# Performance work log

Measured on AMD Instinct MI355X. Metric: run time of the kernel, lower is better.

Reference implementation:

```python
import jax, jax.numpy as jnp
import numpy as np

MID = 16
HEADS = 8
HEAD_DIM = MID // HEADS  # 2
EPS = 1e-5


def posembed(length, dim):
    # get_posembed_linear: sin-cos 1D positional embedding
    pos = jnp.arange(length, dtype=jnp.float32)
    omega = jnp.arange(dim // 2, dtype=jnp.float32) / (dim / 2.0)
    omega = 1.0 / (10000.0 ** omega)
    out = pos[:, None] * omega[None, :]  # [L, dim//2]
    return jnp.concatenate([jnp.sin(out), jnp.cos(out)], axis=1)  # [L, dim]


def layernorm(x, g, b):
    m = x.mean(-1, keepdims=True)
    v = ((x - m) ** 2).mean(-1, keepdims=True)
    return (x - m) * jax.lax.rsqrt(v + EPS) * g + b


def conv2d(x, w, b):
    # NCHW 3x3 SAME conv
    y = jax.lax.conv_general_dilated(x, w, (1, 1), 'SAME',
                                     dimension_numbers=('NCHW', 'OIHW', 'NCHW'))
    return y + b[None, :, None, None]


def attention(x, wq, wk, wv, wo, bo):
    # diffusers Attention: self-attn, no qkv bias, out bias
    B, S, C = x.shape
    q = (x @ wq.T).reshape(B, S, HEADS, HEAD_DIM)
    k = (x @ wk.T).reshape(B, S, HEADS, HEAD_DIM)
    v = (x @ wv.T).reshape(B, S, HEADS, HEAD_DIM)
    scale = 1.0 / np.sqrt(HEAD_DIM).astype(np.float32)
    scores = jnp.einsum('bshd,bthd->bhst', q, k) * scale
    p = jax.nn.softmax(scores, axis=-1)
    o = jnp.einsum('bhst,bthd->bshd', p, v).reshape(B, S, C)
    return o @ wo.T + bo


def setup_inputs() -> dict:
    key = jax.random.key(0)
    ks = jax.random.split(key, 24)

    def n(k, shape, s=0.05):
        return jax.random.normal(k, shape, dtype=jnp.float32) * s

    b, f, h, w, c = 2, 16, 64, 64, 16
    inp = {
        'hidden_states': n(ks[0], (b, f, h, w, c), 1.0),
        'ref_stats': n(ks[1], (b, f, h, w, c), 1.0),
        'emb': n(ks[2], (b, 512), 1.0),
        'conv_in_w': n(ks[3], (MID, c, 3, 3)),
        'conv_in_b': jnp.zeros((MID,), jnp.float32),
        'emb1_w': n(ks[4], (MID, 512)),
        'emb1_b': jnp.zeros((MID,), jnp.float32),
        'emb2_w': n(ks[5], (MID, MID)),
        'emb2_b': jnp.zeros((MID,), jnp.float32),
        'wqx': n(ks[6], (MID, MID)), 'wkx': n(ks[7], (MID, MID)),
        'wvx': n(ks[8], (MID, MID)), 'wox': n(ks[9], (MID, MID)),
        'box': jnp.zeros((MID,), jnp.float32),
        'wqy': n(ks[10], (MID, MID)), 'wky': n(ks[11], (MID, MID)),
        'wvy': n(ks[12], (MID, MID)), 'woy': n(ks[13], (MID, MID)),
        'boy': jnp.zeros((MID,), jnp.float32),
        'wqt': n(ks[14], (MID, MID)), 'wkt': n(ks[15], (MID, MID)),
        'wvt': n(ks[16], (MID, MID)), 'wot': n(ks[17], (MID, MID)),
        'bot': jnp.zeros((MID,), jnp.float32),
        'norm_g': jnp.ones((MID,), jnp.float32),
        'norm_b': jnp.zeros((MID,), jnp.float32),
        'proj_w': n(ks[18], (c, MID, 3, 3)),  # zero_module in torch; random here so grads flow
        'proj_b': jnp.zeros((c,), jnp.float32),
    }
    return inp


def reference(hidden_states, ref_stats, emb,
              conv_in_w, conv_in_b, emb1_w, emb1_b, emb2_w, emb2_b,
              wqx, wkx, wvx, wox, box,
              wqy, wky, wvy, woy, boy,
              wqt, wkt, wvt, wot, bot,
              norm_g, norm_b, proj_w, proj_b):
    b, f, h, w, c = hidden_states.shape

    # conv stem on (b f) c h w
    x = hidden_states.reshape(b * f, h, w, c).transpose(0, 3, 1, 2)
    x = conv2d(x, conv_in_w, conv_in_b)
    r = ref_stats.reshape(b * f, h, w, c).transpose(0, 3, 1, 2)
    r = conv2d(r, conv_in_w, conv_in_b)

    # TimestepEmbedding: linear -> silu -> linear, broadcast over frames/HW
    e = jax.nn.silu(emb @ emb1_w.T + emb1_b) @ emb2_w.T + emb2_b  # [b, MID]
    r = r + jnp.repeat(e, f, axis=0)[:, :, None, None]

    hs = x.reshape(b, f, MID, h, w).transpose(0, 1, 3, 4, 2)  # b f h w c
    rs = r.reshape(b, f, MID, h, w).transpose(0, 1, 3, 4, 2)

    # row (x) attention: cat along w -> (b f h) 2w c
    cat = jnp.concatenate([hs, rs], axis=3).reshape(b * f * h, 2 * w, MID)
    pe = posembed(2 * w, MID)
    resx = attention(layernorm(cat + pe[None], norm_g, norm_b), wqx, wkx, wvx, wox, box)
    resx = resx[:, :w].reshape(b, f, h, w, MID)

    # column (y) attention: cat along h -> (b f w) 2h c
    cat = jnp.concatenate([resx, rs], axis=2)            # b f 2h w c
    cat = cat.transpose(0, 1, 3, 2, 4).reshape(b * f * w, 2 * h, MID)
    pe = posembed(2 * h, MID)
    resy = attention(layernorm(cat + pe[None], norm_g, norm_b), wqy, wky, wvy, woy, boy)
    resy = resy[:, :h].reshape(b, f, w, h, MID).transpose(0, 1, 3, 2, 4)

    # temporal (t) attention: cat along f -> (b h w) 2f c
    cat = jnp.concatenate([resy, rs], axis=1)            # b 2f h w c
    cat = cat.transpose(0, 2, 3, 1, 4).reshape(b * h * w, 2 * f, MID)
    pe = posembed(2 * f, MID)
    rest = attention(layernorm(cat + pe[None], norm_g, norm_b), wqt, wkt, wvt, wot, bot)
    rest = rest[:, :f].reshape(b, h, w, f, MID).transpose(0, 3, 4, 1, 2).reshape(b * f, MID, h, w)

    out = conv2d(rest, proj_w, proj_b)  # (b f) c h w
    return hidden_states + out.reshape(b, f, c, h, w).transpose(0, 1, 3, 4, 2)
```

## Files before the change

### kernel.cpp

```cpp
#include <hip/hip_runtime.h>
#include <hip/hip_bf16.h>

typedef __hip_bfloat16 bf16;

__device__ __forceinline__ float b2f(bf16 x) { return __bfloat162float(x); }

#define BB   2
#define FF   16
#define HH   64
#define WW   64
#define CC   16
#define NIMG (BB*FF)
#define PIX  (HH*WW)
#define IMGSZ (PIX*CC)

#define QSCALE_LOG2E 1.0201394f

__device__ __forceinline__ void ld16bf(const bf16* p, float* x) {
    const uint4* p4 = reinterpret_cast<const uint4*>(p);
    uint4 u0 = p4[0], u1 = p4[1];
    unsigned uu[8] = {u0.x, u0.y, u0.z, u0.w, u1.x, u1.y, u1.z, u1.w};
    #pragma unroll
    for (int k = 0; k < 8; ++k) {
        union { unsigned u; float f; } lo, hi;
        lo.u = uu[k] << 16;
        hi.u = uu[k] & 0xffff0000u;
        x[2 * k] = lo.f;
        x[2 * k + 1] = hi.f;
    }
}
__device__ __forceinline__ void st16bf(bf16* p, const float* x) {
    union { bf16 h[16]; uint4 u[2]; } o;
    #pragma unroll
    for (int k = 0; k < 16; ++k) o.h[k] = __float2bfloat16(x[k]);
    uint4* p4 = reinterpret_cast<uint4*>(p);
    p4[0] = o.u[0];
    p4[1] = o.u[1];
}

__device__ __forceinline__ void ld16f(const float* p, float* x) {
    const float4* p4 = reinterpret_cast<const float4*>(p);
    #pragma unroll
    for (int q = 0; q < 4; ++q) {
        float4 v = p4[q];
        x[4 * q] = v.x; x[4 * q + 1] = v.y; x[4 * q + 2] = v.z; x[4 * q + 3] = v.w;
    }
}
__device__ __forceinline__ void st16f(float* p, const float* x) {
    float4* p4 = reinterpret_cast<float4*>(p);
    #pragma unroll
    for (int q = 0; q < 4; ++q)
        p4[q] = make_float4(x[4 * q], x[4 * q + 1], x[4 * q + 2], x[4 * q + 3]);
}

__device__ __forceinline__ unsigned packbf2(float a, float b) {
    union { bf16 h[2]; unsigned u; } pk;
    pk.h[0] = __float2bfloat16(a);
    pk.h[1] = __float2bfloat16(b);
    return pk.u;
}

__global__ __launch_bounds__(256) void conv_in_kernel(
    const float* __restrict__ hid, const float* __restrict__ ref,
    const float* __restrict__ cw, const float* __restrict__ cb,
    const float* __restrict__ emb,
    const float* __restrict__ e1w, const float* __restrict__ e1b,
    const float* __restrict__ e2w, const float* __restrict__ e2b,
    bf16* __restrict__ A, bf16* __restrict__ R)
{
    __shared__ float wl[9 * 256];
    __shared__ float bl[16];
    __shared__ float hl[16];
    __shared__ float el[16];
    int t = threadIdx.x;
    {
        int ic = t >> 4, oc = t & 15;
        #pragma unroll
        for (int k = 0; k < 9; ++k)
            wl[k * 256 + t] = cw[(oc * 16 + ic) * 9 + k];
    }
    if (t < 16) bl[t] = cb[t];

    int gid  = blockIdx.x * 256 + t;
    int wi   = gid & 63;
    int hi   = (gid >> 6) & 63;
    int img2 = gid >> 12;
    int isref = img2 >> 5;
    int img  = img2 & 31;
    int bi   = img >> 4;

    if (isref) {
        if (t < 16) {
            float acc = e1b[t];
            const float* er = emb + bi * 512;
            const float* wr = e1w + t * 512;
            for (int k = 0; k < 512; ++k) acc = fmaf(er[k], wr[k], acc);
            hl[t] = acc / (1.f + __expf(-acc));
        }
        __syncthreads();
        if (t < 16) {
            float acc = e2b[t];
            #pragma unroll
            for (int k = 0; k < 16; ++k) acc = fmaf(hl[k], e2w[t * 16 + k], acc);
            el[t] = acc;
        }
    }
    __syncthreads();

    const float* inp = (isref ? ref : hid) + (size_t)img * IMGSZ;
    float acc[16];
    #pragma unroll
    for (int oc = 0; oc < 16; ++oc)
        acc[oc] = bl[oc] + (isref ? el[oc] : 0.f);

    for (int ky = 0; ky < 3; ++ky) {
        int y = hi + ky - 1;
        if ((unsigned)y >= 64u) continue;
        for (int kx = 0; kx < 3; ++kx) {
            int x = wi + kx - 1;
            if ((unsigned)x >= 64u) continue;
            float xv[16];
            ld16f(inp + (((y << 6) + x) << 4), xv);
            const float* wt = &wl[(ky * 3 + kx) * 256];
            #pragma unroll
            for (int ic = 0; ic < 16; ++ic) {
                #pragma unroll
                for (int oc = 0; oc < 16; ++oc)
                    acc[oc] = fmaf(xv[ic], wt[ic * 16 + oc], acc[oc]);
            }
        }
    }
    bf16* op = (isref ? R : A) + ((size_t)(img * PIX + (hi << 6) + wi) << 4);
    st16bf(op, acc);
}

template<int S, int SEQPB>
__global__ __launch_bounds__(256, 5) void attn_kernel(
    bf16* __restrict__ A, const bf16* __restrict__ R,
    int d2, int str1, int str2, int tokStride,
    const float* __restrict__ wq, const float* __restrict__ wk,
    const float* __restrict__ wv, const float* __restrict__ wo,
    const float* __restrict__ bo, const float* __restrict__ gw,
    const float* __restrict__ bw)
{
    constexpr int HS = S / 2;
    constexpr int KQ = S / 2;
    constexpr int ITEMS = 256 / SEQPB;
    constexpr int KROW = 20;
    constexpr int QROW = 20;

    __shared__ float wql[256], wkl[256], wvl[256], wolT[256];
    __shared__ float bol[16], gl[16], blw[16];
    __shared__ __align__(16) float kL[SEQPB * S * KROW];
    __shared__ __align__(16) float vL[SEQPB * S * KROW];
    __shared__ __align__(16) float qoL[SEQPB * HS * QROW];
    __shared__ int   bases[SEQPB];

    int t = threadIdx.x;
    wql[t] = wq[t] * QSCALE_LOG2E;
    wkl[t] = wk[t];
    wvl[t] = wv[t];
    wolT[(t & 15) * 16 + (t >> 4)] = wo[t];
    if (t < 16) { bol[t] = bo[t]; gl[t] = gw[t]; blw[t] = bw[t]; }
    if (t < SEQPB) {
        int seq = blockIdx.x * SEQPB + t;
        bases[t] = (seq / d2) * str1 + (seq % d2) * str2;
    }
    __syncthreads();

    {
        int pair = t >> 1, halfT = t & 1;
        int sq = pair / S, i = pair % S;
        const bf16* src = (i < HS)
            ? (A + bases[sq] + (size_t)i * tokStride)
            : (R + bases[sq] + (size_t)(i - HS) * tokStride);
        float x[16];
        ld16bf(src, x);
        const float om[8] = {1.f, 0.31622776601683794f, 0.1f, 0.031622776601683794f,
                             0.01f, 0.0031622776601683794f, 0.001f, 0.00031622776601683794f};
        float fi = (float)i;
        #pragma unroll
        for (int k = 0; k < 8; ++k) {
            float a = fi * om[k];
            x[k]     += __sinf(a);
            x[k + 8] += __cosf(a);
        }
        float m = 0.f;
        #pragma unroll
        for (int c = 0; c < 16; ++c) m += x[c];
        m *= (1.f / 16.f);
        float var = 0.f;
        #pragma unroll
        for (int c = 0; c < 16; ++c) { float d = x[c] - m; var = fmaf(d, d, var); }
        var *= (1.f / 16.f);
        float rs = rsqrtf(var + 1e-5f);
        float xn[16];
        #pragma unroll
        for (int c = 0; c < 16; ++c) xn[c] = (x[c] - m) * rs * gl[c] + blw[c];

        int db = halfT * 8;
        float qv[8], kv[8], vv[8];
        #pragma unroll
        for (int dd = 0; dd < 8; ++dd) {
            int d = db + dd;
            float aq = 0.f, ak = 0.f, av = 0.f;
            #pragma unroll
            for (int c = 0; c < 16; ++c) {
                aq = fmaf(xn[c], wql[d * 16 + c], aq);
                ak = fmaf(xn[c], wkl[d * 16 + c], ak);
                av = fmaf(xn[c], wvl[d * 16 + c], av);
            }
            qv[dd] = aq; kv[dd] = ak; vv[dd] = av;
        }
        float* kr = &kL[(sq * S + i) * KROW + db];
        float* vr = &vL[(sq * S + i) * KROW + db];
        reinterpret_cast<float4*>(kr)[0] = make_float4(kv[0], kv[1], kv[2], kv[3]);
        reinterpret_cast<float4*>(kr)[1] = make_float4(kv[4], kv[5], kv[6], kv[7]);
        reinterpret_cast<float4*>(vr)[0] = make_float4(vv[0], vv[1], vv[2], vv[3]);
        reinterpret_cast<float4*>(vr)[1] = make_float4(vv[4], vv[5], vv[6], vv[7]);
        if (i < HS) {
            float* qrow = &qoL[(sq * HS + i) * QROW + db];
            reinterpret_cast<float4*>(qrow)[0] = make_float4(qv[0], qv[1], qv[2], qv[3]);
            reinterpret_cast<float4*>(qrow)[1] = make_float4(qv[4], qv[5], qv[6], qv[7]);
        }
    }
    __syncthreads();

    int sq2 = t / ITEMS;
    int r   = t % ITEMS;
    int qg  = r >> 4;
    int hd  = (r >> 1) & 7;
    int half = r & 1;
    {
        float q0[4], q1[4], l[4], a0[4], a1[4];
        #pragma unroll
        for (int qq = 0; qq < 4; ++qq) {
            float2 qv = *reinterpret_cast<const float2*>(
                &qoL[(sq2 * HS + qg * 4 + qq) * QROW + 2 * hd]);
            q0[qq] = qv.x;
            q1[qq] = qv.y;
            l[qq] = 0.f; a0[qq] = 0.f; a1[qq] = 0.f;
        }
        const float* kp = &kL[(sq2 * S + half) * KROW + 2 * hd];
        const float* vp = &vL[(sq2 * S + half) * KROW + 2 * hd];
        #pragma unroll
        for (int jj = 0; jj < KQ; ++jj) {
            float2 kj = *reinterpret_cast<const float2*>(kp + jj * 2 * KROW);
            float2 vj = *reinterpret_cast<const float2*>(vp + jj * 2 * KROW);
            #pragma unroll
            for (int qq = 0; qq < 4; ++qq) {
                float s = fmaf(q0[qq], kj.x, q1[qq] * kj.y);
                float p = __builtin_amdgcn_exp2f(s);
                l[qq] += p;
                a0[qq] = fmaf(p, vj.x, a0[qq]);
                a1[qq] = fmaf(p, vj.y, a1[qq]);
            }
        }
        #pragma unroll
        for (int qq = 0; qq < 4; ++qq) {
            l[qq]  += __shfl_xor(l[qq], 1);
            a0[qq] += __shfl_xor(a0[qq], 1);
            a1[qq] += __shfl_xor(a1[qq], 1);
        }
        __syncthreads();
        if (half == 0) {
            #pragma unroll
            for (int qq = 0; qq < 4; ++qq) {
                float inv = 1.f / l[qq];
                *reinterpret_cast<float2*>(
                    &qoL[(sq2 * HS + qg * 4 + qq) * QROW + 2 * hd]) =
                    make_float2(a0[qq] * inv, a1[qq] * inv);
            }
        }
    }
    __syncthreads();

    #pragma unroll
    for (int rep = 0; rep < 2; ++rep) {
        int idx = t + rep * 256;
        int sq3 = idx / (HS * 8);
        int rr  = idx % (HS * 8);
        int tok = rr >> 3;
        int cp  = rr & 7;
        const float* orow = &qoL[(sq3 * HS + tok) * QROW];
        float acc0 = bol[2 * cp], acc1 = bol[2 * cp + 1];
        #pragma unroll
        for (int d = 0; d < 16; ++d) {
            acc0 = fmaf(orow[d], wolT[d * 16 + 2 * cp], acc0);
            acc1 = fmaf(orow[d], wolT[d * 16 + 2 * cp + 1], acc1);
        }
        *reinterpret_cast<unsigned*>(
            A + bases[sq3] + (size_t)tok * tokStride + 2 * cp) =
            packbf2(acc0, acc1);
    }
}

__global__ __launch_bounds__(256) void conv_out_kernel(
    const bf16* __restrict__ A, const float* __restrict__ hid,
    const float* __restrict__ pw, const float* __restrict__ pb,
    float* __restrict__ out)
{
    __shared__ float wl[9 * 256];
    __shared__ float bl[16];
    int t = threadIdx.x;
    {
        int ic = t >> 4, oc = t & 15;
        #pragma unroll
        for (int k = 0; k < 9; ++k)
            wl[k * 256 + t] = pw[(oc * 16 + ic) * 9 + k];
    }
    if (t < 16) bl[t] = pb[t];
    __syncthreads();

    int gid = blockIdx.x * 256 + t;
    int wi = gid & 63, hi = (gid >> 6) & 63;
    int img = gid >> 12;
    const bf16* inp = A + ((size_t)img << 16);
    float acc[16];
    #pragma unroll
    for (int oc = 0; oc < 16; ++oc) acc[oc] = bl[oc];

    for (int ky = 0; ky < 3; ++ky) {
        int y = hi + ky - 1;
        if ((unsigned)y >= 64u) continue;
        for (int kx = 0; kx < 3; ++kx) {
            int x = wi + kx - 1;
            if ((unsigned)x >= 64u) continue;
            float xv[16];
            ld16bf(inp + (((y << 6) + x) << 4), xv);
            const float* wt = &wl[(ky * 3 + kx) * 256];
            #pragma unroll
            for (int ic = 0; ic < 16; ++ic) {
                #pragma unroll
                for (int oc = 0; oc < 16; ++oc)
                    acc[oc] = fmaf(xv[ic], wt[ic * 16 + oc], acc[oc]);
            }
        }
    }
    size_t off = ((size_t)gid) << 4;
    float hv[16];
    ld16f(hid + off, hv);
    float res[16];
    #pragma unroll
    for (int k = 0; k < 16; ++k) res[k] = acc[k] + hv[k];
    st16f(out + off, res);
}

extern "C" void kernel_launch(void* const* d_in, const int* in_sizes, int n_in,
                              void* d_out, int out_size, void* d_ws, size_t ws_size,
                              hipStream_t stream) {
    const float* hid  = (const float*)d_in[0];
    const float* ref  = (const float*)d_in[1];
    const float* emb  = (const float*)d_in[2];
    const float* ciw  = (const float*)d_in[3];
    const float* cib  = (const float*)d_in[4];
    const float* e1w  = (const float*)d_in[5];
    const float* e1b  = (const float*)d_in[6];
    const float* e2w  = (const float*)d_in[7];
    const float* e2b  = (const float*)d_in[8];
    const float* wqx  = (const float*)d_in[9];
    const float* wkx  = (const float*)d_in[10];
    const float* wvx  = (const float*)d_in[11];
    const float* wox  = (const float*)d_in[12];
    const float* box_ = (const float*)d_in[13];
    const float* wqy  = (const float*)d_in[14];
    const float* wky  = (const float*)d_in[15];
    const float* wvy  = (const float*)d_in[16];
    const float* woy  = (const float*)d_in[17];
    const float* boy  = (const float*)d_in[18];
    const float* wqt  = (const float*)d_in[19];
    const float* wkt  = (const float*)d_in[20];
    const float* wvt  = (const float*)d_in[21];
    const float* wot  = (const float*)d_in[22];
    const float* bot  = (const float*)d_in[23];
    const float* ng   = (const float*)d_in[24];
    const float* nb   = (const float*)d_in[25];
    const float* pjw  = (const float*)d_in[26];
    const float* pjb  = (const float*)d_in[27];

    bf16* A = (bf16*)d_ws;
    bf16* R = (bf16*)d_out;

    conv_in_kernel<<<(2 * NIMG * PIX) / 256, 256, 0, stream>>>(
        hid, ref, ciw, cib, emb, e1w, e1b, e2w, e2b, A, R);

    attn_kernel<128, 1><<<BB * FF * HH, 256, 0, stream>>>(
        A, R, 1, WW * CC, 0, CC, wqx, wkx, wvx, wox, box_, ng, nb);
    attn_kernel<128, 1><<<BB * FF * WW, 256, 0, stream>>>(
        A, R, WW, IMGSZ, CC, WW * CC, wqy, wky, wvy, woy, boy, ng, nb);
    attn_kernel<32, 4><<<(BB * HH * WW) / 4, 256, 0, stream>>>(
        A, R, HH * WW, FF * IMGSZ, CC, IMGSZ, wqt, wkt, wvt, wot, bot, ng, nb);

    conv_out_kernel<<<(NIMG * PIX) / 256, 256, 0, stream>>>(A, hid, pjw, pjb, (float*)d_out);
}
```

Before: 278.6 us.

## Store K/V as packed bf16 in LDS and batch two column sequences per block

K and V tiles in shared memory are now stored as packed bf16 pairs instead of fp32, halving their LDS footprint, and are unpacked in the attention inner loop. The column attention now processes two sequences per block, with one token per thread for the projection stage and interleaved sequence/token indexing. Launch-bound occupancy hints become a per-instantiation template parameter. sin/cos is fused into one sincos call. The smaller LDS footprint is meant to raise occupancy, at the cost of extra unpack work and bf16 rounding of K/V.

Result: no change. 274.3 us (median of 2 runs) (-1.5%).

```diff
diff --git a/kernel.cpp b/kernel.cpp
--- a/kernel.cpp
+++ b/kernel.cpp
@@ -134,8 +134,8 @@
     st16bf(op, acc);
 }
 
-template<int S, int SEQPB>
-__global__ __launch_bounds__(256, 5) void attn_kernel(
+template<int S, int SEQPB, int MINW>
+__global__ __launch_bounds__(256, MINW) void attn_kernel(
     bf16* __restrict__ A, const bf16* __restrict__ R,
     int d2, int str1, int str2, int tokStride,
     const float* __restrict__ wq, const float* __restrict__ wk,
@@ -143,18 +143,23 @@
     const float* __restrict__ bo, const float* __restrict__ gw,
     const float* __restrict__ bw)
 {
-    constexpr int HS = S / 2;
-    constexpr int KQ = S / 2;
+    constexpr int HS  = S / 2;
+    constexpr int KQ  = S / 2;
+    constexpr int TPT = 256 / (SEQPB * S);
     constexpr int ITEMS = 256 / SEQPB;
-    constexpr int KROW = 20;
+    constexpr int NQG = ITEMS / 16;
+    constexpr int QB  = HS / NQG;
+    constexpr int KROW = 10;
     constexpr int QROW = 20;
+    constexpr int LSQ = (SEQPB == 1) ? 0 : ((SEQPB == 2) ? 1 : 2);
+    constexpr int NW3 = SEQPB * HS * 8 / 256;
 
     __shared__ float wql[256], wkl[256], wvl[256], wolT[256];
     __shared__ float bol[16], gl[16], blw[16];
-    __shared__ __align__(16) float kL[SEQPB * S * KROW];
-    __shared__ __align__(16) float vL[SEQPB * S * KROW];
+    __shared__ __align__(16) unsigned kU[SEQPB * S * KROW];
+    __shared__ __align__(16) unsigned vU[SEQPB * S * KROW];
     __shared__ __align__(16) float qoL[SEQPB * HS * QROW];
-    __shared__ int   bases[SEQPB];
+    __shared__ int bases[SEQPB];
 
     int t = threadIdx.x;
     wql[t] = wq[t] * QSCALE_LOG2E;
@@ -169,8 +174,18 @@
     __syncthreads();
 
     {
-        int pair = t >> 1, halfT = t & 1;
-        int sq = pair / S, i = pair % S;
+        int tokIdx, sq, i, db, ndim;
+        if (TPT == 2) {
+            tokIdx = t >> 1;
+            db = (t & 1) * 8;
+            ndim = 8;
+        } else {
+            tokIdx = t;
+            db = 0;
+            ndim = 16;
+        }
+        sq = tokIdx & (SEQPB - 1);
+        i  = tokIdx >> LSQ;
         const bf16* src = (i < HS)
             ? (A + bases[sq] + (size_t)i * tokStride)
             : (R + bases[sq] + (size_t)(i - HS) * tokStride);
@@ -181,9 +196,10 @@
         float fi = (float)i;
         #pragma unroll
         for (int k = 0; k < 8; ++k) {
-            float a = fi * om[k];
-            x[k]     += __sinf(a);
-            x[k + 8] += __cosf(a);
+            float sv, cv;
+            __sincosf(fi * om[k], &sv, &cv);
+            x[k]     += sv;
+            x[k + 8] += cv;
         }
         float m = 0.f;
         #pragma unroll
@@ -198,10 +214,10 @@
         #pragma unroll
         for (int c = 0; c < 16; ++c) xn[c] = (x[c] - m) * rs * gl[c] + blw[c];
 
-        int db = halfT * 8;
-        float qv[8], kv[8], vv[8];
-        #pragma unroll
-        for (int dd = 0; dd < 8; ++dd) {
+        float qv[16], kv[16], vv[16];
+        #pragma unroll
+        for (int dd = 0; dd < 16; ++dd) {
+            if (dd >= ndim) break;
             int d = db + dd;
             float aq = 0.f, ak = 0.f, av = 0.f;
             #pragma unroll
@@ -212,16 +228,22 @@
             }
             qv[dd] = aq; kv[dd] = ak; vv[dd] = av;
         }
-        float* kr = &kL[(sq * S + i) * KROW + db];
-        float* vr = &vL[(sq * S + i) * KROW + db];
-        reinterpret_cast<float4*>(kr)[0] = make_float4(kv[0], kv[1], kv[2], kv[3]);
-        reinterpret_cast<float4*>(kr)[1] = make_float4(kv[4], kv[5], kv[6], kv[7]);
-        reinterpret_cast<float4*>(vr)[0] = make_float4(vv[0], vv[1], vv[2], vv[3]);
-        reinterpret_cast<float4*>(vr)[1] = make_float4(vv[4], vv[5], vv[6], vv[7]);
+        int row = (sq * S + i) * KROW + (db >> 1);
+        uint2* kr = reinterpret_cast<uint2*>(&kU[row]);
+        uint2* vr = reinterpret_cast<uint2*>(&vU[row]);
+        #pragma unroll
+        for (int e = 0; e < ndim / 4; ++e) {
+            kr[e] = make_uint2(packbf2(kv[4 * e], kv[4 * e + 1]),
+                               packbf2(kv[4 * e + 2], kv[4 * e + 3]));
+            vr[e] = make_uint2(packbf2(vv[4 * e], vv[4 * e + 1]),
+                               packbf2(vv[4 * e + 2], vv[4 * e + 3]));
+        }
         if (i < HS) {
             float* qrow = &qoL[(sq * HS + i) * QROW + db];
-            reinterpret_cast<float4*>(qrow)[0] = make_float4(qv[0], qv[1], qv[2], qv[3]);
-            reinterpret_cast<float4*>(qrow)[1] = make_float4(qv[4], qv[5], qv[6], qv[7]);
+            #pragma unroll
+            for (int e = 0; e < ndim / 4; ++e)
+                reinterpret_cast<float4*>(qrow)[e] =
+                    make_float4(qv[4 * e], qv[4 * e + 1], qv[4 * e + 2], qv[4 * e + 3]);
         }
     }
     __syncthreads();
@@ -232,32 +254,35 @@
     int hd  = (r >> 1) & 7;
     int half = r & 1;
     {
-        float q0[4], q1[4], l[4], a0[4], a1[4];
-        #pragma unroll
-        for (int qq = 0; qq < 4; ++qq) {
+        float q0[QB], q1[QB], l[QB], a0[QB], a1[QB];
+        #pragma unroll
+        for (int qq = 0; qq < QB; ++qq) {
             float2 qv = *reinterpret_cast<const float2*>(
-                &qoL[(sq2 * HS + qg * 4 + qq) * QROW + 2 * hd]);
+                &qoL[(sq2 * HS + qg * QB + qq) * QROW + 2 * hd]);
             q0[qq] = qv.x;
             q1[qq] = qv.y;
             l[qq] = 0.f; a0[qq] = 0.f; a1[qq] = 0.f;
         }
-        const float* kp = &kL[(sq2 * S + half) * KROW + 2 * hd];
-        const float* vp = &vL[(sq2 * S + half) * KROW + 2 * hd];
-        #pragma unroll
+        const unsigned* kp = &kU[(sq2 * S + half) * KROW + hd];
+        const unsigned* vp = &vU[(sq2 * S + half) * KROW + hd];
+        #pragma unroll 8
         for (int jj = 0; jj < KQ; ++jj) {
-            float2 kj = *reinterpret_cast<const float2*>(kp + jj * 2 * KROW);
-            float2 vj = *reinterpret_cast<const float2*>(vp + jj * 2 * KROW);
-            #pragma unroll
-            for (int qq = 0; qq < 4; ++qq) {
-                float s = fmaf(q0[qq], kj.x, q1[qq] * kj.y);
+            unsigned ku = kp[jj * 2 * KROW];
+            unsigned vu = vp[jj * 2 * KROW];
+            union { unsigned u; float f; } k0, k1, v0, v1;
+            k0.u = ku << 16; k1.u = ku & 0xffff0000u;
+            v0.u = vu << 16; v1.u = vu & 0xffff0000u;
+            #pragma unroll
+            for (int qq = 0; qq < QB; ++qq) {
+                float s = fmaf(q0[qq], k0.f, q1[qq] * k1.f);
                 float p = __builtin_amdgcn_exp2f(s);
                 l[qq] += p;
-                a0[qq] = fmaf(p, vj.x, a0[qq]);
-                a1[qq] = fmaf(p, vj.y, a1[qq]);
+                a0[qq] = fmaf(p, v0.f, a0[qq]);
+                a1[qq] = fmaf(p, v1.f, a1[qq]);
             }
         }
         #pragma unroll
-        for (int qq = 0; qq < 4; ++qq) {
+        for (int qq = 0; qq < QB; ++qq) {
             l[qq]  += __shfl_xor(l[qq], 1);
             a0[qq] += __shfl_xor(a0[qq], 1);
             a1[qq] += __shfl_xor(a1[qq], 1);
@@ -265,10 +290,10 @@
         __syncthreads();
         if (half == 0) {
             #pragma unroll
-            for (int qq = 0; qq < 4; ++qq) {
+            for (int qq = 0; qq < QB; ++qq) {
                 float inv = 1.f / l[qq];
                 *reinterpret_cast<float2*>(
-                    &qoL[(sq2 * HS + qg * 4 + qq) * QROW + 2 * hd]) =
+                    &qoL[(sq2 * HS + qg * QB + qq) * QROW + 2 * hd]) =
                     make_float2(a0[qq] * inv, a1[qq] * inv);
             }
         }
@@ -276,12 +301,12 @@
     __syncthreads();
 
     #pragma unroll
-    for (int rep = 0; rep < 2; ++rep) {
+    for (int rep = 0; rep < NW3; ++rep) {
         int idx = t + rep * 256;
-        int sq3 = idx / (HS * 8);
-        int rr  = idx % (HS * 8);
-        int tok = rr >> 3;
-        int cp  = rr & 7;
+        int cp  = idx & 7;
+        int g   = idx >> 3;
+        int sq3 = g & (SEQPB - 1);
+        int tok = g >> LSQ;
         const float* orow = &qoL[(sq3 * HS + tok) * QROW];
         float acc0 = bol[2 * cp], acc1 = bol[2 * cp + 1];
         #pragma unroll
@@ -384,11 +409,11 @@
     conv_in_kernel<<<(2 * NIMG * PIX) / 256, 256, 0, stream>>>(
         hid, ref, ciw, cib, emb, e1w, e1b, e2w, e2b, A, R);
 
-    attn_kernel<128, 1><<<BB * FF * HH, 256, 0, stream>>>(
+    attn_kernel<128, 1, 8><<<BB * FF * HH, 256, 0, stream>>>(
         A, R, 1, WW * CC, 0, CC, wqx, wkx, wvx, wox, box_, ng, nb);
-    attn_kernel<128, 1><<<BB * FF * WW, 256, 0, stream>>>(
+    attn_kernel<128, 2, 4><<<(BB * FF * WW) / 2, 256, 0, stream>>>(
         A, R, WW, IMGSZ, CC, WW * CC, wqy, wky, wvy, woy, boy, ng, nb);
-    attn_kernel<32, 4><<<(BB * HH * WW) / 4, 256, 0, stream>>>(
+    attn_kernel<32, 4, 8><<<(BB * HH * WW) / 4, 256, 0, stream>>>(
         A, R, HH * WW, FF * IMGSZ, CC, IMGSZ, wqt, wkt, wvt, wot, bot, ng, nb);
 
     conv_out_kernel<<<(NIMG * PIX) / 256, 256, 0, stream>>>(A, hid, pjw, pjb, (float*)d_out);
```
